# Kernel tuning notes

Hardware: AMD Instinct MI355X
Metric: run time of the kernel (lower is better)

Reference implementation:

```python
import jax, jax.numpy as jnp
import numpy as np

N, E, IN_DIM, HID, HEADS, LAYERS, NUM_STORES = 50000, 800000, 64, 128, 16, 3, 50
DH = HID // HEADS  # per-head dim = 8
EPS = 1e-5


def setup_inputs() -> dict:
    key = jax.random.key(0)
    ks = iter(jax.random.split(key, 40))
    def nrm(shape, scale):
        return jax.random.normal(next(ks), shape, dtype=jnp.float32) * scale
    inp = {}
    inp['x'] = jax.random.normal(next(ks), (N, IN_DIM), dtype=jnp.float32)
    inp['edge_index'] = jax.random.randint(next(ks), (2, E), 0, N, dtype=jnp.int32)
    inp['edge_weight'] = jax.random.uniform(next(ks), (E, 1), dtype=jnp.float32)
    inp['store_mask'] = jax.random.randint(next(ks), (N,), 0, NUM_STORES, dtype=jnp.int32)
    # input_proj: Linear + GELU + LayerNorm
    inp['in_W'] = nrm((IN_DIM, HID), IN_DIM ** -0.5)
    inp['in_b'] = jnp.zeros((HID,), jnp.float32)
    inp['in_g'] = jnp.ones((HID,), jnp.float32)
    inp['in_beta'] = jnp.zeros((HID,), jnp.float32)
    # 3 stacked GATv2 layers (stacked leading dim = layer)
    s = HID ** -0.5
    inp['gat_Wl'] = nrm((LAYERS, HID, HID), s)
    inp['gat_bl'] = jnp.zeros((LAYERS, HID), jnp.float32)
    inp['gat_Wr'] = nrm((LAYERS, HID, HID), s)
    inp['gat_br'] = jnp.zeros((LAYERS, HID), jnp.float32)
    inp['gat_We'] = nrm((LAYERS, 1, HID), 1.0)
    inp['gat_att'] = nrm((LAYERS, HEADS, DH), DH ** -0.5)
    inp['gat_bias'] = jnp.zeros((LAYERS, HID), jnp.float32)
    inp['blk_g'] = jnp.ones((LAYERS, HID), jnp.float32)
    inp['blk_b'] = jnp.zeros((LAYERS, HID), jnp.float32)
    # per-store context gate + final norm
    inp['ctx_W'] = nrm((HID, HID), s)
    inp['ctx_b'] = jnp.zeros((HID,), jnp.float32)
    inp['fin_g'] = jnp.ones((HID,), jnp.float32)
    inp['fin_b'] = jnp.zeros((HID,), jnp.float32)
    return inp


def layernorm(x, g, b):
    mu = jnp.mean(x, axis=-1, keepdims=True)
    v = jnp.mean((x - mu) ** 2, axis=-1, keepdims=True)
    return (x - mu) * jax.lax.rsqrt(v + EPS) * g + b


def gatv2_layer(x, src, dst, ea, Wl, bl, Wr, br, We, att, bias):
    # x: [N, HID]; src/dst: [Et]; ea: [Et, 1]
    n = x.shape[0]
    xl = (x @ Wl + bl).reshape(n, HEADS, DH)   # source transform
    xr = (x @ Wr + br).reshape(n, HEADS, DH)   # target transform
    ee = (ea @ We).reshape(-1, HEADS, DH)      # edge-attr embedding
    e = jax.nn.leaky_relu(xl[src] + xr[dst] + ee, 0.2)  # [Et, H, D]
    logit = jnp.einsum('ehd,hd->eh', e, att)             # [Et, H]
    # segment softmax over incoming edges of each target node
    mx = jax.ops.segment_max(logit, dst, num_segments=n)
    p = jnp.exp(logit - mx[dst])
    Z = jax.ops.segment_sum(p, dst, num_segments=n)
    alpha = p / (Z[dst] + 1e-16)
    msg = alpha[:, :, None] * xl[src]                    # [Et, H, D]
    agg = jax.ops.segment_sum(msg, dst, num_segments=n)  # [N, H, D]
    return agg.reshape(n, HEADS * DH) + bias


def forward(x, edge_index, edge_weight, store_mask, in_W, in_b, in_g, in_beta,
            gat_Wl, gat_bl, gat_Wr, gat_br, gat_We, gat_att, gat_bias,
            blk_g, blk_b, ctx_W, ctx_b, fin_g, fin_b):
    n = x.shape[0]
    h = layernorm(jax.nn.gelu(x @ in_W + in_b, approximate=False), in_g, in_beta)
    src, dst = edge_index[0], edge_index[1]
    # PyG add_self_loops with fill_value='mean': per-target mean of incoming edge attrs
    deg = jax.ops.segment_sum(jnp.ones(src.shape, h.dtype), dst, num_segments=n)
    loop_attr = jax.ops.segment_sum(edge_weight, dst, num_segments=n) / jnp.maximum(deg, 1.0)[:, None]
    loops = jnp.arange(n, dtype=src.dtype)
    srcf = jnp.concatenate([src, loops])
    dstf = jnp.concatenate([dst, loops])
    eaf = jnp.concatenate([edge_weight, loop_attr], axis=0)
    for l in range(LAYERS):  # residual block: post-norm residual around conv
        m = gatv2_layer(h, srcf, dstf, eaf, gat_Wl[l], gat_bl[l], gat_Wr[l], gat_br[l],
                        gat_We[l], gat_att[l], gat_bias[l])
        h = layernorm(h + m, blk_g[l], blk_b[l])
    # per-store segmented mean -> sigmoid gate -> scatter back
    cnt = jax.ops.segment_sum(jnp.ones((n,), h.dtype), store_mask, num_segments=NUM_STORES)
    means = jax.ops.segment_sum(h, store_mask, num_segments=NUM_STORES) / jnp.maximum(cnt, 1.0)[:, None]
    gate = jax.nn.sigmoid(means @ ctx_W + ctx_b)
    h = h + (gate * means)[store_mask]
    return layernorm(h, fin_g, fin_b)


def reference(x, edge_index, edge_weight, store_mask, in_W, in_b, in_g, in_beta,
              gat_Wl, gat_bl, gat_Wr, gat_br, gat_We, gat_att, gat_bias,
              blk_g, blk_b, ctx_W, ctx_b, fin_g, fin_b):
    return forward(x, edge_index, edge_weight, store_mask, in_W, in_b, in_g, in_beta,
                   gat_Wl, gat_bl, gat_Wr, gat_br, gat_We, gat_att, gat_bias,
                   blk_g, blk_b, ctx_W, ctx_b, fin_g, fin_b)
```

## Files before the change

kernel.cpp:

```cpp
#include <hip/hip_runtime.h>
#include <math.h>

#define NN 50000
#define EE 800000
#define ET (EE + NN)
#define HID 128
#define NSTORE 50
#define NBL 196
#define CNT_B 3125
#define XCV_B 3125
#define WCV_B 192
#define IWC_B 32
#define SCT_B 3321
#define GEMB 391
#define SSB 512

typedef unsigned short ushort_t;
typedef unsigned long long u64;
typedef __attribute__((ext_vector_type(8))) short bf8;
typedef __attribute__((ext_vector_type(4))) float f4;
typedef __attribute__((ext_vector_type(2))) float f2;
typedef __attribute__((ext_vector_type(4))) unsigned int u4;

__device__ __forceinline__ ushort_t f2b(float f) {
    union { float f; unsigned int i; } v; v.f = f;
    unsigned int r = (v.i + 0x7fffu + ((v.i >> 16) & 1u)) >> 16;
    return (ushort_t)r;
}
__device__ __forceinline__ f2 b2f2v(unsigned int u) {
    union { unsigned int i; float f; } lo, hi;
    lo.i = u << 16; hi.i = u & 0xffff0000u;
    f2 r; r.x = lo.f; r.y = hi.f; return r;
}
__device__ __forceinline__ unsigned int pk2(float lo, float hi) {
    return (unsigned int)f2b(lo) | ((unsigned int)f2b(hi) << 16);
}
__device__ __forceinline__ f2 max2(f2 a, f2 b) {
#if __has_builtin(__builtin_elementwise_max)
    return __builtin_elementwise_max(a, b);
#else
    f2 r; r.x = fmaxf(a.x, b.x); r.y = fmaxf(a.y, b.y); return r;
#endif
}

__global__ __launch_bounds__(256) void k_build(const int* __restrict__ ei, const float* __restrict__ ew,
                                               const float* __restrict__ x, const float* __restrict__ inW,
                                               const float* __restrict__ gWl, const float* __restrict__ gWr,
                                               ushort_t* __restrict__ xb, ushort_t* __restrict__ inWt,
                                               ushort_t* __restrict__ Wlt, ushort_t* __restrict__ Wrt,
                                               u64* __restrict__ packed, int* __restrict__ rank) {
    int b = blockIdx.x, t = threadIdx.x;
    if (b < CNT_B) {
        int i = b * 256 + t;
        int dst = ei[EE + i];
        unsigned int wfix = __float2uint_rn(ew[i] * 16777216.0f);
        u64 old = atomicAdd(&packed[dst], (1ULL << 44) | (u64)wfix);
        rank[i] = (int)(old >> 44);
        return;
    }
    if (b < CNT_B + XCV_B) {
        int i = ((b - CNT_B) * 256 + t) * 4;
        f4 v = *(const f4*)(x + i);
        uint2 p; p.x = pk2(v.x, v.y); p.y = pk2(v.z, v.w);
        *(uint2*)(xb + i) = p;
        return;
    }
    if (b < CNT_B + XCV_B + WCV_B) {
        int i = (b - CNT_B - XCV_B) * 256 + t;
        int l = i >> 14, r = i & 16383, nn2 = r >> 7, k = r & 127;
        Wlt[i] = f2b(gWl[(size_t)l * 16384 + k * 128 + nn2]);
        Wrt[i] = f2b(gWr[(size_t)l * 16384 + k * 128 + nn2]);
        return;
    }
    {
        int i = (b - CNT_B - XCV_B - WCV_B) * 256 + t;
        int c = i >> 6, k = i & 63;
        inWt[i] = f2b(inW[k * 128 + c]);
    }
}

__global__ __launch_bounds__(256) void k_inproj(const ushort_t* __restrict__ A,
                                                const ushort_t* __restrict__ Wt,
                                                const float* __restrict__ bias,
                                                const float* __restrict__ g,
                                                const float* __restrict__ be,
                                                ushort_t* __restrict__ hb) {
    const int K = 64;
    __shared__ float s1[2][128], s2[2][128];
    int lane = threadIdx.x & 63, w = threadIdx.x >> 6;
    int rw = w >> 1, cw = w & 1;
    int q = lane >> 4, l16 = lane & 15;
    int row0 = blockIdx.x * 128 + rw * 64;
    int col0 = cw * 64;
    bf8 z; for (int t = 0; t < 8; ++t) z[t] = 0;

    bf8 bfr[2][4];
#pragma unroll
    for (int kk = 0; kk < 2; ++kk)
#pragma unroll
        for (int j = 0; j < 4; ++j)
            bfr[kk][j] = *(const bf8*)(Wt + (size_t)(col0 + j * 16 + l16) * K + kk * 32 + q * 8);

    f4 acc[4][4];
#pragma unroll
    for (int i = 0; i < 4; ++i)
#pragma unroll
        for (int j = 0; j < 4; ++j) acc[i][j] = (f4)(0.f);

#pragma unroll
    for (int kk = 0; kk < 2; ++kk) {
        bf8 af[4];
#pragma unroll
        for (int i = 0; i < 4; ++i) {
            int r = row0 + i * 16 + l16;
            af[i] = (r < NN) ? *(const bf8*)(A + (size_t)r * K + kk * 32 + q * 8) : z;
        }
#pragma unroll
        for (int i = 0; i < 4; ++i)
#pragma unroll
            for (int j = 0; j < 4; ++j)
                acc[i][j] = __builtin_amdgcn_mfma_f32_16x16x32_bf16(af[i], bfr[kk][j], acc[i][j], 0, 0, 0);
    }
#pragma unroll
    for (int i = 0; i < 4; ++i) {
#pragma unroll
        for (int j = 0; j < 4; ++j) {
            float bv = bias[col0 + j * 16 + l16];
#pragma unroll
            for (int r = 0; r < 4; ++r) {
                float v = acc[i][j][r] + bv;
                v = 0.5f * v * (1.f + erff(v * 0.70710678118654752f));
                acc[i][j][r] = v;
            }
        }
    }
#pragma unroll
    for (int i = 0; i < 4; ++i) {
#pragma unroll
        for (int r = 0; r < 4; ++r) {
            float sm = acc[i][0][r] + acc[i][1][r] + acc[i][2][r] + acc[i][3][r];
            float sq = acc[i][0][r] * acc[i][0][r] + acc[i][1][r] * acc[i][1][r]
                     + acc[i][2][r] * acc[i][2][r] + acc[i][3][r] * acc[i][3][r];
#pragma unroll
            for (int k = 1; k < 16; k <<= 1) { sm += __shfl_xor(sm, k); sq += __shfl_xor(sq, k); }
            if (l16 == 0) {
                int rl = rw * 64 + i * 16 + q * 4 + r;
                s1[cw][rl] = sm; s2[cw][rl] = sq;
            }
        }
    }
    __syncthreads();
#pragma unroll
    for (int i = 0; i < 4; ++i) {
#pragma unroll
        for (int r = 0; r < 4; ++r) {
            int rl = rw * 64 + i * 16 + q * 4 + r;
            int gr = blockIdx.x * 128 + rl;
            if (gr >= NN) continue;
            float sm = s1[0][rl] + s1[1][rl];
            float sq = s2[0][rl] + s2[1][rl];
            float mu = sm * (1.f / 128.f);
            float var = sq * (1.f / 128.f) - mu * mu;
            float rinv = rsqrtf(var + 1e-5f);
#pragma unroll
            for (int j = 0; j < 4; ++j) {
                int gc = col0 + j * 16 + l16;
                float v = (acc[i][j][r] - mu) * rinv * g[gc] + be[gc];
                hb[(size_t)gr * HID + gc] = f2b(v);
            }
        }
    }
}

__global__ __launch_bounds__(256) void k_psum(const u64* __restrict__ packed, int* __restrict__ bsum) {
    int t = threadIdx.x, bidx = blockIdx.x;
    int i = bidx * 256 + t;
    int v = (i < NN) ? (int)(packed[i] >> 44) + 1 : 0;
#pragma unroll
    for (int d = 1; d < 64; d <<= 1) v += __shfl_xor(v, d);
    __shared__ int ws4[4];
    if ((t & 63) == 0) ws4[t >> 6] = v;
    __syncthreads();
    if (t == 0) bsum[bidx] = ws4[0] + ws4[1] + ws4[2] + ws4[3];
}

__global__ __launch_bounds__(256) void k_scanb(const int* __restrict__ bsum,
                                               int* __restrict__ bbase, int* __restrict__ offs) {
    __shared__ int s[256];
    int t = threadIdx.x;
    int v = (t < NBL) ? bsum[t] : 0;
    s[t] = v;
    __syncthreads();
    for (int d = 1; d < 256; d <<= 1) {
        int u = (t >= d) ? s[t - d] : 0;
        __syncthreads();
        s[t] += u;
        __syncthreads();
    }
    if (t < NBL) bbase[t] = s[t] - v;
    if (t == 0) offs[NN] = ET;
}

__global__ __launch_bounds__(256) void k_offs(const u64* __restrict__ packed,
                                              const int* __restrict__ bbase, int* __restrict__ offs) {
    __shared__ int wsum4[4];
    int t = threadIdx.x, bidx = blockIdx.x;
    int i = bidx * 256 + t;
    int v = (i < NN) ? (int)(packed[i] >> 44) + 1 : 0;
    int lane = t & 63, w = t >> 6;
    int sc = v;
#pragma unroll
    for (int d = 1; d < 64; d <<= 1) {
        int u = __shfl_up(sc, d);
        if (lane >= d) sc += u;
    }
    if (lane == 63) wsum4[w] = sc;
    __syncthreads();
    int wo = 0;
    for (int k = 0; k < w; ++k) wo += wsum4[k];
    if (i < NN) offs[i] = bbase[bidx] + wo + sc - v;
}

__global__ __launch_bounds__(256) void k_gemm2(const ushort_t* __restrict__ A,
                                               const ushort_t* __restrict__ Wt0,
                                               const ushort_t* __restrict__ Wt1,
                                               const float* __restrict__ b0,
                                               const float* __restrict__ b1,
                                               ushort_t* __restrict__ o0,
                                               ushort_t* __restrict__ o1, int n,
                                               const int* __restrict__ ei,
                                               const float* __restrict__ ew,
                                               const int* __restrict__ offs,
                                               const u64* __restrict__ packed,
                                               const int* __restrict__ rank,
                                               int2* __restrict__ csr) {
    int bid = blockIdx.x;
    if (bid >= 2 * GEMB) {
        int i = (bid - 2 * GEMB) * 256 + threadIdx.x;
        if (i < EE) {
            int src = ei[i], dst = ei[EE + i];
            int pos = offs[dst] + rank[i];
            int2 v; v.x = src << 8; v.y = __float_as_int(ew[i]);
            csr[pos] = v;
        } else if (i < ET) {
            int nd = i - EE;
            u64 p = packed[nd];
            int deg = (int)(p >> 44);
            float wsf = (float)(p & ((1ULL << 44) - 1)) * (1.0f / 16777216.0f);
            float la = wsf / fmaxf((float)deg, 1.0f);
            int pos = offs[nd + 1] - 1;
            int2 v; v.x = nd << 8; v.y = __float_as_int(la);
            csr[pos] = v;
        }
        return;
    }
    const int K = 128;
    int by = (bid >= GEMB) ? 1 : 0;
    int bx = by ? bid - GEMB : bid;
    const ushort_t* Wt = by ? Wt1 : Wt0;
    const float* bias = by ? b1 : b0;
    ushort_t* outb = by ? o1 : o0;
    int lane = threadIdx.x & 63, w = threadIdx.x >> 6;
    int rw = w >> 1, cw = w & 1;
    int q = lane >> 4, l16 = lane & 15;
    int row0 = bx * 128 + rw * 64;
    int col0 = cw * 64;
    bf8 z; for (int t = 0; t < 8; ++t) z[t] = 0;

    bf8 bfr[4][4];
#pragma unroll
    for (int kk = 0; kk < 4; ++kk)
#pragma unroll
        for (int j = 0; j < 4; ++j)
            bfr[kk][j] = *(const bf8*)(Wt + (size_t)(col0 + j * 16 + l16) * K + kk * 32 + q * 8);

    f4 acc[4][4];
#pragma unroll
    for (int i = 0; i < 4; ++i)
#pragma unroll
        for (int j = 0; j < 4; ++j) acc[i][j] = (f4)(0.f);

#pragma unroll
    for (int kk = 0; kk < 4; ++kk) {
        bf8 af[4];
#pragma unroll
        for (int i = 0; i < 4; ++i) {
            int r = row0 + i * 16 + l16;
            af[i] = (r < n) ? *(const bf8*)(A + (size_t)r * K + kk * 32 + q * 8) : z;
        }
#pragma unroll
        for (int i = 0; i < 4; ++i)
#pragma unroll
            for (int j = 0; j < 4; ++j)
                acc[i][j] = __builtin_amdgcn_mfma_f32_16x16x32_bf16(af[i], bfr[kk][j], acc[i][j], 0, 0, 0);
    }
#pragma unroll
    for (int i = 0; i < 4; ++i) {
        int gr0 = row0 + i * 16 + q * 4;
#pragma unroll
        for (int j = 0; j < 4; ++j) {
            int gc = col0 + j * 16 + l16;
            float bv = bias[gc];
#pragma unroll
            for (int r = 0; r < 4; ++r) {
                int gr = gr0 + r;
                if (gr < n) outb[(size_t)gr * HID + gc] = f2b(acc[i][j][r] + bv);
            }
        }
    }
}

__global__ __launch_bounds__(256) void k_attn(const ushort_t* __restrict__ xl,
                                              const ushort_t* __restrict__ xr,
                                              ushort_t* __restrict__ hb,
                                              const int* __restrict__ offs,
                                              const int2* __restrict__ csr,
                                              const float* __restrict__ We,
                                              const float* __restrict__ att,
                                              const float* __restrict__ gbias,
                                              const float* __restrict__ g,
                                              const float* __restrict__ b) {
    int wid = (blockIdx.x * 256 + threadIdx.x) >> 6;
    int lane = threadIdx.x & 63;
    if (wid >= NN) return;
    int hd = lane & 15;
    int grp = lane >> 4;
    int dbase = hd * 8;
    int db2 = hd * 16;
    size_t base = (size_t)wid * HID;

    f2 xr2[4], at2[4], we2[4];
    {
        u4 uxr = *(const u4*)(xr + base + dbase);
        xr2[0] = b2f2v(uxr.x); xr2[1] = b2f2v(uxr.y);
        xr2[2] = b2f2v(uxr.z); xr2[3] = b2f2v(uxr.w);
        f4 a0 = *(const f4*)(att + dbase), a1 = *(const f4*)(att + dbase + 4);
        at2[0].x = a0.x; at2[0].y = a0.y; at2[1].x = a0.z; at2[1].y = a0.w;
        at2[2].x = a1.x; at2[2].y = a1.y; at2[3].x = a1.z; at2[3].y = a1.w;
        f4 w0 = *(const f4*)(We + dbase), w1 = *(const f4*)(We + dbase + 4);
        we2[0].x = w0.x; we2[0].y = w0.y; we2[1].x = w0.z; we2[1].y = w0.w;
        we2[2].x = w1.x; we2[2].y = w1.y; we2[3].x = w1.z; we2[3].y = w1.w;
    }
    int p0 = offs[wid], p1 = offs[wid + 1];
    float Z = 0.f;
    f2 acc2[4];
#pragma unroll
    for (int q = 0; q < 4; ++q) { acc2[q].x = 0.f; acc2[q].y = 0.f; }

#define LOADQ(UX, EA, VM)                                                      \
    {                                                                          \
        int ei_ = e + grp;                                                     \
        VM = (ei_ < p1);                                                       \
        int2 m2_ = csr[VM ? ei_ : (p1 - 1)];                                   \
        EA = __int_as_float(m2_.y);                                            \
        UX = *(const u4*)((const char*)xl + (unsigned)m2_.x + db2);            \
    }

#define COMPQ(UX, EA, VM)                                                      \
    {                                                                          \
        f2 x2_[4];                                                             \
        x2_[0] = b2f2v(UX.x); x2_[1] = b2f2v(UX.y);                            \
        x2_[2] = b2f2v(UX.z); x2_[3] = b2f2v(UX.w);                            \
        f2 lg2_; lg2_.x = 0.f; lg2_.y = 0.f;                                   \
        _Pragma("unroll")                                                      \
        for (int q_ = 0; q_ < 4; ++q_) {                                       \
            f2 t_ = (x2_[q_] + xr2[q_]) + EA * we2[q_];                        \
            t_ = max2(t_, t_ * 0.2f);                                          \
            lg2_ += at2[q_] * t_;                                              \
        }                                                                      \
        float w_ = VM ? __expf(lg2_.x + lg2_.y) : 0.f;                         \
        Z += w_;                                                               \
        _Pragma("unroll")                                                      \
        for (int q_ = 0; q_ < 4; ++q_) acc2[q_] += w_ * x2_[q_];               \
    }

    {
        u4 uxA, uxB; float eaA, eaB; bool vA, vB;
        int e = p0;
        LOADQ(uxA, eaA, vA)
        e += 4;
        while (e < p1) {
            LOADQ(uxB, eaB, vB)
            e += 4;
            COMPQ(uxA, eaA, vA)
            if (e >= p1) { COMPQ(uxB, eaB, vB) goto redux; }
            LOADQ(uxA, eaA, vA)
            e += 4;
            COMPQ(uxB, eaB, vB)
        }
        COMPQ(uxA, eaA, vA)
    }
redux:;
#undef LOADQ
#undef COMPQ

    Z += __shfl_xor(Z, 16); Z += __shfl_xor(Z, 32);
#pragma unroll
    for (int q = 0; q < 4; ++q) {
        acc2[q].x += __shfl_xor(acc2[q].x, 16);
        acc2[q].x += __shfl_xor(acc2[q].x, 32);
        acc2[q].y += __shfl_xor(acc2[q].y, 16);
        acc2[q].y += __shfl_xor(acc2[q].y, 32);
    }
    float inv = 1.f / (Z + 1e-16f);
    float acc[8] = {acc2[0].x, acc2[0].y, acc2[1].x, acc2[1].y,
                    acc2[2].x, acc2[2].y, acc2[3].x, acc2[3].y};

    u4 uh = *(const u4*)(hb + base + dbase);
    f2 hr0 = b2f2v(uh.x), hr1 = b2f2v(uh.y), hr2 = b2f2v(uh.z), hr3 = b2f2v(uh.w);
    float hres[8] = {hr0.x, hr0.y, hr1.x, hr1.y, hr2.x, hr2.y, hr3.x, hr3.y};
    f4 gb0 = *(const f4*)(gbias + dbase), gb1 = *(const f4*)(gbias + dbase + 4);
    float gb8[8] = {gb0.x, gb0.y, gb0.z, gb0.w, gb1.x, gb1.y, gb1.z, gb1.w};
    float o[8], sm = 0.f, sq = 0.f;
#pragma unroll
    for (int q = 0; q < 8; ++q) {
        o[q] = acc[q] * inv + gb8[q] + hres[q];
        sm += o[q]; sq += o[q] * o[q];
    }
#pragma unroll
    for (int k = 1; k < 16; k <<= 1) { sm += __shfl_xor(sm, k); sq += __shfl_xor(sq, k); }
    float mu = sm * (1.f / 128.f);
    float var = sq * (1.f / 128.f) - mu * mu;
    float rinv = rsqrtf(var + 1e-5f);
    f4 g0 = *(const f4*)(g + dbase), g1 = *(const f4*)(g + dbase + 4);
    float g8[8] = {g0.x, g0.y, g0.z, g0.w, g1.x, g1.y, g1.z, g1.w};
    f4 b0 = *(const f4*)(b + dbase), b1 = *(const f4*)(b + dbase + 4);
    float b8[8] = {b0.x, b0.y, b0.z, b0.w, b1.x, b1.y, b1.z, b1.w};
    float v8[8];
#pragma unroll
    for (int q = 0; q < 8; ++q) v8[q] = (o[q] - mu) * rinv * g8[q] + b8[q];
    if (grp == 0) {
        u4 hu;
        hu.x = pk2(v8[0], v8[1]); hu.y = pk2(v8[2], v8[3]);
        hu.z = pk2(v8[4], v8[5]); hu.w = pk2(v8[6], v8[7]);
        *(u4*)(hb + base + dbase) = hu;
    }
}

__global__ __launch_bounds__(256) void k_store_sum(const ushort_t* __restrict__ hb,
                                                   const int* __restrict__ mask,
                                                   float* __restrict__ psums,
                                                   int* __restrict__ pcnts) {
    __shared__ float ls[NSTORE * HID];
    __shared__ int lc[NSTORE];
    int t = threadIdx.x, bidx = blockIdx.x;
    for (int i = t; i < NSTORE * HID; i += 256) ls[i] = 0.f;
    if (t < NSTORE) lc[t] = 0;
    __syncthreads();
    int wid = bidx * 4 + (t >> 6);
    int lane = t & 63;
    int nw = SSB * 4;
    int d0 = lane * 2;
    for (int node = wid; node < NN; node += nw) {
        int s = mask[node];
        unsigned int hv = ((const unsigned int*)(hb + (size_t)node * HID))[lane];
        f2 v = b2f2v(hv);
        atomicAdd(&ls[s * HID + d0], v.x);
        atomicAdd(&ls[s * HID + d0 + 1], v.y);
        if (lane == 0) atomicAdd(&lc[s], 1);
    }
    __syncthreads();
    for (int i = t; i < NSTORE * HID; i += 256) psums[(size_t)bidx * (NSTORE * HID) + i] = ls[i];
    if (t < NSTORE) pcnts[bidx * NSTORE + t] = lc[t];
}

__global__ __launch_bounds__(256) void k_gate(const float* __restrict__ psums,
                                              const int* __restrict__ pcnts,
                                              const float* __restrict__ ctxW,
                                              const float* __restrict__ ctxb,
                                              float* __restrict__ gm) {
    __shared__ float h1[HID];
    __shared__ float mloc[HID];
    __shared__ int cw4[4];
    int s = blockIdx.x, t = threadIdx.x;
    int d = t & 127, half = t >> 7;
    float s0 = 0.f, s1 = 0.f, s2 = 0.f, s3 = 0.f;
    for (int b = half * 4; b < SSB; b += 8) {
        s0 += psums[(size_t)(b + 0) * (NSTORE * HID) + s * HID + d];
        s1 += psums[(size_t)(b + 1) * (NSTORE * HID) + s * HID + d];
        s2 += psums[(size_t)(b + 2) * (NSTORE * HID) + s * HID + d];
        s3 += psums[(size_t)(b + 3) * (NSTORE * HID) + s * HID + d];
    }
    float sum = (s0 + s1) + (s2 + s3);
    int c = pcnts[t * NSTORE + s] + pcnts[(t + 256) * NSTORE + s];
#pragma unroll
    for (int k = 1; k < 64; k <<= 1) c += __shfl_xor(c, k);
    if ((t & 63) == 0) cw4[t >> 6] = c;
    if (half) h1[d] = sum;
    __syncthreads();
    if (half == 0) {
        float tot = sum + h1[d];
        float cnt = fmaxf((float)(cw4[0] + cw4[1] + cw4[2] + cw4[3]), 1.f);
        mloc[d] = tot / cnt;
    }
    __syncthreads();
    if (half == 0) {
        float acc = ctxb[d];
        for (int j = 0; j < HID; ++j) acc += mloc[j] * ctxW[j * HID + d];
        float gate = 1.f / (1.f + __expf(-acc));
        gm[s * HID + d] = gate * mloc[d];
    }
}

__global__ __launch_bounds__(256) void k_final(const ushort_t* __restrict__ hb,
                                               const int* __restrict__ mask,
                                               const float* __restrict__ gm,
                                               const float* __restrict__ g,
                                               const float* __restrict__ b,
                                               float* __restrict__ out) {
    int wid = (blockIdx.x * 256 + threadIdx.x) >> 6;
    int lane = threadIdx.x & 63;
    if (wid >= NN) return;
    size_t base = (size_t)wid * HID;
    int s = mask[wid];
    int d0 = lane * 2, d1 = d0 + 1;
    unsigned int hv = ((const unsigned int*)(hb + base))[lane];
    f2 hvv = b2f2v(hv);
    float v0 = hvv.x + gm[s * HID + d0];
    float v1 = hvv.y + gm[s * HID + d1];
    float sm = v0 + v1, sq = v0 * v0 + v1 * v1;
#pragma unroll
    for (int k = 1; k < 64; k <<= 1) { sm += __shfl_xor(sm, k); sq += __shfl_xor(sq, k); }
    float mu = sm * (1.f / 128.f);
    float var = sq * (1.f / 128.f) - mu * mu;
    float r = rsqrtf(var + 1e-5f);
    out[base + d0] = (v0 - mu) * r * g[d0] + b[d0];
    out[base + d1] = (v1 - mu) * r * g[d1] + b[d1];
}

extern "C" void kernel_launch(void* const* d_in, const int* in_sizes, int n_in,
                              void* d_out, int out_size, void* d_ws, size_t ws_size,
                              hipStream_t stream) {
    const float* x      = (const float*)d_in[0];
    const int*   ei     = (const int*)d_in[1];
    const float* ew     = (const float*)d_in[2];
    const int*   smask  = (const int*)d_in[3];
    const float* inW    = (const float*)d_in[4];
    const float* inb    = (const float*)d_in[5];
    const float* ing    = (const float*)d_in[6];
    const float* inbeta = (const float*)d_in[7];
    const float* gWl    = (const float*)d_in[8];
    const float* gbl    = (const float*)d_in[9];
    const float* gWr    = (const float*)d_in[10];
    const float* gbr    = (const float*)d_in[11];
    const float* gWe    = (const float*)d_in[12];
    const float* gatt   = (const float*)d_in[13];
    const float* gbias  = (const float*)d_in[14];
    const float* blkg   = (const float*)d_in[15];
    const float* blkb   = (const float*)d_in[16];
    const float* ctxW   = (const float*)d_in[17];
    const float* ctxb   = (const float*)d_in[18];
    const float* fing   = (const float*)d_in[19];
    const float* finb   = (const float*)d_in[20];
    float* out = (float*)d_out;

    float* ws = (float*)d_ws;
    size_t o = 0;
    int2*     csr    = (int2*)(ws + o);     o += (size_t)ET * 2;
    float*    gm     = ws + o;              o += NSTORE * HID;
    int*      offs   = (int*)(ws + o);      o += 50004;
    int*      rank   = (int*)(ws + o);      o += EE;
    ushort_t* xb     = (ushort_t*)(ws + o); o += (size_t)NN * 64 / 2;
    ushort_t* hb     = (ushort_t*)(ws + o); o += (size_t)NN * HID / 2;
    ushort_t* xlb    = (ushort_t*)(ws + o); o += (size_t)NN * HID / 2;
    ushort_t* xrb    = (ushort_t*)(ws + o); o += (size_t)NN * HID / 2;
    ushort_t* inWt   = (ushort_t*)(ws + o); o += 128 * 64 / 2;
    ushort_t* Wlt    = (ushort_t*)(ws + o); o += 3 * 128 * 128 / 2;
    ushort_t* Wrt    = (ushort_t*)(ws + o); o += 3 * 128 * 128 / 2;
    int*      bsum   = (int*)(ws + o);      o += 256;
    int*      bbase  = (int*)(ws + o);      o += 256;
    float*    psums  = ws + o;              o += (size_t)SSB * NSTORE * HID;
    int*      pcnts  = (int*)(ws + o);      o += SSB * NSTORE;
    if (o & 1) ++o;
    float*    zbase  = ws + o;
    u64*      packed = (u64*)(ws + o);      o += (size_t)NN * 2;
    size_t zbytes = (size_t)(NN * 2) * 4;

    hipMemsetAsync((void*)zbase, 0, zbytes, stream);

    const int WB = NN / 4;

    k_build<<<CNT_B + XCV_B + WCV_B + IWC_B, 256, 0, stream>>>(ei, ew, x, inW, gWl, gWr,
                                                               xb, inWt, Wlt, Wrt, packed, rank);
    k_inproj<<<GEMB, 256, 0, stream>>>(xb, inWt, inb, ing, inbeta, hb);
    k_psum<<<NBL, 256, 0, stream>>>(packed, bsum);
    k_scanb<<<1, 256, 0, stream>>>(bsum, bbase, offs);
    k_offs<<<NBL, 256, 0, stream>>>(packed, bbase, offs);

    for (int l = 0; l < 3; ++l) {
        int nb = 2 * GEMB + (l == 0 ? SCT_B : 0);
        k_gemm2<<<nb, 256, 0, stream>>>(hb, Wlt + (size_t)l * HID * HID, Wrt + (size_t)l * HID * HID,
                                        gbl + l * HID, gbr + l * HID, xlb, xrb, NN,
                                        ei, ew, offs, packed, rank, csr);
        k_attn<<<WB, 256, 0, stream>>>(xlb, xrb, hb, offs, csr,
                                       gWe + l * HID, gatt + l * HID, gbias + l * HID,
                                       blkg + l * HID, blkb + l * HID);
    }

    k_store_sum<<<SSB, 256, 0, stream>>>(hb, smask, psums, pcnts);
    k_gate<<<NSTORE, 256, 0, stream>>>(psums, pcnts, ctxW, ctxb, gm);
    k_final<<<WB, 256, 0, stream>>>(hb, smask, gm, fing, finb, out);
}
```

Before: 507.6 us.

## Batch CSR record loads via lane shuffles and make attention kernel persistent

The attention kernel becomes grid-stride persistent with a fixed grid, and its launch bounds now request 8 waves per SIMD. Each wave loads up to 64 CSR records for its node in a single coalesced load and hands them out with shuffles. It then issues up to four gathers of neighbour features before computing, instead of one CSR load followed by a dependent gather. This removes the serial CSR-then-gather latency chain and increases memory-level parallelism. The costs are more registers, a fallback loop for nodes with degree above 64, and a grid-stride loop that may balance load unevenly.

```diff
diff --git a/kernel.cpp b/kernel.cpp
--- a/kernel.cpp
+++ b/kernel.cpp
@@ -14,6 +14,7 @@
 #define SCT_B 3321
 #define GEMB 391
 #define SSB 512
+#define ATT_B 2048
 
 typedef unsigned short ushort_t;
 typedef unsigned long long u64;
@@ -310,30 +311,25 @@
     }
 }
 
-__global__ __launch_bounds__(256) void k_attn(const ushort_t* __restrict__ xl,
-                                              const ushort_t* __restrict__ xr,
-                                              ushort_t* __restrict__ hb,
-                                              const int* __restrict__ offs,
-                                              const int2* __restrict__ csr,
-                                              const float* __restrict__ We,
-                                              const float* __restrict__ att,
-                                              const float* __restrict__ gbias,
-                                              const float* __restrict__ g,
-                                              const float* __restrict__ b) {
-    int wid = (blockIdx.x * 256 + threadIdx.x) >> 6;
+__global__ __launch_bounds__(256, 8) void k_attn(const ushort_t* __restrict__ xl,
+                                                 const ushort_t* __restrict__ xr,
+                                                 ushort_t* __restrict__ hb,
+                                                 const int* __restrict__ offs,
+                                                 const int2* __restrict__ csr,
+                                                 const float* __restrict__ We,
+                                                 const float* __restrict__ att,
+                                                 const float* __restrict__ gbias,
+                                                 const float* __restrict__ g,
+                                                 const float* __restrict__ b) {
     int lane = threadIdx.x & 63;
-    if (wid >= NN) return;
+    int wslot = __builtin_amdgcn_readfirstlane(threadIdx.x >> 6);
     int hd = lane & 15;
     int grp = lane >> 4;
     int dbase = hd * 8;
     int db2 = hd * 16;
-    size_t base = (size_t)wid * HID;
-
-    f2 xr2[4], at2[4], we2[4];
+
+    f2 at2[4], we2[4];
     {
-        u4 uxr = *(const u4*)(xr + base + dbase);
-        xr2[0] = b2f2v(uxr.x); xr2[1] = b2f2v(uxr.y);
-        xr2[2] = b2f2v(uxr.z); xr2[3] = b2f2v(uxr.w);
         f4 a0 = *(const f4*)(att + dbase), a1 = *(const f4*)(att + dbase + 4);
         at2[0].x = a0.x; at2[0].y = a0.y; at2[1].x = a0.z; at2[1].y = a0.w;
         at2[2].x = a1.x; at2[2].y = a1.y; at2[3].x = a1.z; at2[3].y = a1.w;
@@ -341,23 +337,37 @@
         we2[0].x = w0.x; we2[0].y = w0.y; we2[1].x = w0.z; we2[1].y = w0.w;
         we2[2].x = w1.x; we2[2].y = w1.y; we2[3].x = w1.z; we2[3].y = w1.w;
     }
-    int p0 = offs[wid], p1 = offs[wid + 1];
-    float Z = 0.f;
-    f2 acc2[4];
-#pragma unroll
-    for (int q = 0; q < 4; ++q) { acc2[q].x = 0.f; acc2[q].y = 0.f; }
-
-#define LOADQ(UX, EA, VM)                                                      \
+
+    for (int wid = blockIdx.x * 4 + wslot; wid < NN; wid += ATT_B * 4) {
+        size_t base = (size_t)wid * HID;
+        f2 xr2[4];
+        {
+            u4 uxr = *(const u4*)(xr + base + dbase);
+            xr2[0] = b2f2v(uxr.x); xr2[1] = b2f2v(uxr.y);
+            xr2[2] = b2f2v(uxr.z); xr2[3] = b2f2v(uxr.w);
+        }
+        int p0 = offs[wid], p1 = offs[wid + 1];
+        int deg = p1 - p0;
+        int nmain = deg > 64 ? 64 : deg;
+        int2 rec = csr[p0 + ((lane < deg) ? lane : deg - 1)];
+
+        float Z = 0.f;
+        f2 acc2[4];
+#pragma unroll
+        for (int q = 0; q < 4; ++q) { acc2[q].x = 0.f; acc2[q].y = 0.f; }
+
+#define ISSUE(K, UX, EA)                                                       \
     {                                                                          \
-        int ei_ = e + grp;                                                     \
-        VM = (ei_ < p1);                                                       \
-        int2 m2_ = csr[VM ? ei_ : (p1 - 1)];                                   \
-        EA = __int_as_float(m2_.y);                                            \
-        UX = *(const u4*)((const char*)xl + (unsigned)m2_.x + db2);            \
-    }
-
-#define COMPQ(UX, EA, VM)                                                      \
+        int ie_ = e0 + 4 * K + grp;                                            \
+        int is_ = (ie_ < nmain) ? ie_ : 0;                                     \
+        EA = __int_as_float(__shfl(rec.y, is_));                               \
+        int sx_ = __shfl(rec.x, is_);                                          \
+        UX = *(const u4*)((const char*)xl + (unsigned)sx_ + db2);              \
+    }
+
+#define COMP(K, UX, EA)                                                        \
     {                                                                          \
+        bool vm_ = (e0 + 4 * K + grp) < nmain;                                 \
         f2 x2_[4];                                                             \
         x2_[0] = b2f2v(UX.x); x2_[1] = b2f2v(UX.y);                            \
         x2_[2] = b2f2v(UX.z); x2_[3] = b2f2v(UX.w);                            \
@@ -368,72 +378,91 @@
             t_ = max2(t_, t_ * 0.2f);                                          \
             lg2_ += at2[q_] * t_;                                              \
         }                                                                      \
-        float w_ = VM ? __expf(lg2_.x + lg2_.y) : 0.f;                         \
+        float w_ = vm_ ? __expf(lg2_.x + lg2_.y) : 0.f;                        \
         Z += w_;                                                               \
         _Pragma("unroll")                                                      \
         for (int q_ = 0; q_ < 4; ++q_) acc2[q_] += w_ * x2_[q_];               \
     }
 
-    {
-        u4 uxA, uxB; float eaA, eaB; bool vA, vB;
-        int e = p0;
-        LOADQ(uxA, eaA, vA)
-        e += 4;
-        while (e < p1) {
-            LOADQ(uxB, eaB, vB)
-            e += 4;
-            COMPQ(uxA, eaA, vA)
-            if (e >= p1) { COMPQ(uxB, eaB, vB) goto redux; }
-            LOADQ(uxA, eaA, vA)
-            e += 4;
-            COMPQ(uxB, eaB, vB)
-        }
-        COMPQ(uxA, eaA, vA)
-    }
-redux:;
-#undef LOADQ
-#undef COMPQ
-
-    Z += __shfl_xor(Z, 16); Z += __shfl_xor(Z, 32);
-#pragma unroll
-    for (int q = 0; q < 4; ++q) {
-        acc2[q].x += __shfl_xor(acc2[q].x, 16);
-        acc2[q].x += __shfl_xor(acc2[q].x, 32);
-        acc2[q].y += __shfl_xor(acc2[q].y, 16);
-        acc2[q].y += __shfl_xor(acc2[q].y, 32);
-    }
-    float inv = 1.f / (Z + 1e-16f);
-    float acc[8] = {acc2[0].x, acc2[0].y, acc2[1].x, acc2[1].y,
-                    acc2[2].x, acc2[2].y, acc2[3].x, acc2[3].y};
-
-    u4 uh = *(const u4*)(hb + base + dbase);
-    f2 hr0 = b2f2v(uh.x), hr1 = b2f2v(uh.y), hr2 = b2f2v(uh.z), hr3 = b2f2v(uh.w);
-    float hres[8] = {hr0.x, hr0.y, hr1.x, hr1.y, hr2.x, hr2.y, hr3.x, hr3.y};
-    f4 gb0 = *(const f4*)(gbias + dbase), gb1 = *(const f4*)(gbias + dbase + 4);
-    float gb8[8] = {gb0.x, gb0.y, gb0.z, gb0.w, gb1.x, gb1.y, gb1.z, gb1.w};
-    float o[8], sm = 0.f, sq = 0.f;
-#pragma unroll
-    for (int q = 0; q < 8; ++q) {
-        o[q] = acc[q] * inv + gb8[q] + hres[q];
-        sm += o[q]; sq += o[q] * o[q];
-    }
-#pragma unroll
-    for (int k = 1; k < 16; k <<= 1) { sm += __shfl_xor(sm, k); sq += __shfl_xor(sq, k); }
-    float mu = sm * (1.f / 128.f);
-    float var = sq * (1.f / 128.f) - mu * mu;
-    float rinv = rsqrtf(var + 1e-5f);
-    f4 g0 = *(const f4*)(g + dbase), g1 = *(const f4*)(g + dbase + 4);
-    float g8[8] = {g0.x, g0.y, g0.z, g0.w, g1.x, g1.y, g1.z, g1.w};
-    f4 b0 = *(const f4*)(b + dbase), b1 = *(const f4*)(b + dbase + 4);
-    float b8[8] = {b0.x, b0.y, b0.z, b0.w, b1.x, b1.y, b1.z, b1.w};
-    float v8[8];
-#pragma unroll
-    for (int q = 0; q < 8; ++q) v8[q] = (o[q] - mu) * rinv * g8[q] + b8[q];
-    if (grp == 0) {
-        u4 hu;
-        hu.x = pk2(v8[0], v8[1]); hu.y = pk2(v8[2], v8[3]);
-        hu.z = pk2(v8[4], v8[5]); hu.w = pk2(v8[6], v8[7]);
-        *(u4*)(hb + base + dbase) = hu;
+        for (int e0 = 0; e0 < nmain; e0 += 16) {
+            int nr = nmain - e0;
+            u4 uxA, uxB, uxC, uxD;
+            float eaA, eaB, eaC, eaD;
+            ISSUE(0, uxA, eaA)
+            if (nr > 4)  ISSUE(1, uxB, eaB)
+            if (nr > 8)  ISSUE(2, uxC, eaC)
+            if (nr > 12) ISSUE(3, uxD, eaD)
+            COMP(0, uxA, eaA)
+            if (nr > 4)  COMP(1, uxB, eaB)
+            if (nr > 8)  COMP(2, uxC, eaC)
+            if (nr > 12) COMP(3, uxD, eaD)
+        }
+#undef ISSUE
+#undef COMP
+
+        for (int e = p0 + 64; e < p1; e += 4) {
+            int ei_ = e + grp;
+            bool vm_ = ei_ < p1;
+            int2 m2_ = csr[vm_ ? ei_ : p1 - 1];
+            float ea_ = __int_as_float(m2_.y);
+            u4 ux_ = *(const u4*)((const char*)xl + (unsigned)m2_.x + db2);
+            f2 x2_[4];
+            x2_[0] = b2f2v(ux_.x); x2_[1] = b2f2v(ux_.y);
+            x2_[2] = b2f2v(ux_.z); x2_[3] = b2f2v(ux_.w);
+            f2 lg2_; lg2_.x = 0.f; lg2_.y = 0.f;
+#pragma unroll
+            for (int q_ = 0; q_ < 4; ++q_) {
+                f2 t_ = (x2_[q_] + xr2[q_]) + ea_ * we2[q_];
+                t_ = max2(t_, t_ * 0.2f);
+                lg2_ += at2[q_] * t_;
+            }
+            float w_ = vm_ ? __expf(lg2_.x + lg2_.y) : 0.f;
+            Z += w_;
+#pragma unroll
+            for (int q_ = 0; q_ < 4; ++q_) acc2[q_] += w_ * x2_[q_];
+        }
+
+        Z += __shfl_xor(Z, 16); Z += __shfl_xor(Z, 32);
+#pragma unroll
+        for (int q = 0; q < 4; ++q) {
+            acc2[q].x += __shfl_xor(acc2[q].x, 16);
+            acc2[q].x += __shfl_xor(acc2[q].x, 32);
+            acc2[q].y += __shfl_xor(acc2[q].y, 16);
+            acc2[q].y += __shfl_xor(acc2[q].y, 32);
+        }
+        float inv = 1.f / (Z + 1e-16f);
+        float acc[8] = {acc2[0].x, acc2[0].y, acc2[1].x, acc2[1].y,
+                        acc2[2].x, acc2[2].y, acc2[3].x, acc2[3].y};
+
+        u4 uh = *(const u4*)(hb + base + dbase);
+        f2 hr0 = b2f2v(uh.x), hr1 = b2f2v(uh.y), hr2 = b2f2v(uh.z), hr3 = b2f2v(uh.w);
+        float hres[8] = {hr0.x, hr0.y, hr1.x, hr1.y, hr2.x, hr2.y, hr3.x, hr3.y};
+        f4 gb0 = *(const f4*)(gbias + dbase), gb1 = *(const f4*)(gbias + dbase + 4);
+        float gb8[8] = {gb0.x, gb0.y, gb0.z, gb0.w, gb1.x, gb1.y, gb1.z, gb1.w};
+        float o[8], sm = 0.f, sq = 0.f;
+#pragma unroll
+        for (int q = 0; q < 8; ++q) {
+            o[q] = acc[q] * inv + gb8[q] + hres[q];
+            sm += o[q]; sq += o[q] * o[q];
+        }
+#pragma unroll
+        for (int k = 1; k < 16; k <<= 1) { sm += __shfl_xor(sm, k); sq += __shfl_xor(sq, k); }
+        float mu = sm * (1.f / 128.f);
+        float var = sq * (1.f / 128.f) - mu * mu;
+        float rinv = rsqrtf(var + 1e-5f);
+        f4 g0 = *(const f4*)(g + dbase), g1 = *(const f4*)(g + dbase + 4);
+        float g8[8] = {g0.x, g0.y, g0.z, g0.w, g1.x, g1.y, g1.z, g1.w};
+        f4 b0 = *(const f4*)(b + dbase), b1 = *(const f4*)(b + dbase + 4);
+        float b8[8] = {b0.x, b0.y, b0.z, b0.w, b1.x, b1.y, b1.z, b1.w};
+        float v8[8];
+#pragma unroll
+        for (int q = 0; q < 8; ++q) v8[q] = (o[q] - mu) * rinv * g8[q] + b8[q];
+        if (grp == 0) {
+            u4 hu;
+            hu.x = pk2(v8[0], v8[1]); hu.y = pk2(v8[2], v8[3]);
+            hu.z = pk2(v8[4], v8[5]); hu.w = pk2(v8[6], v8[7]);
+            *(u4*)(hb + base + dbase) = hu;
+        }
     }
 }
 
@@ -592,9 +621,9 @@
         k_gemm2<<<nb, 256, 0, stream>>>(hb, Wlt + (size_t)l * HID * HID, Wrt + (size_t)l * HID * HID,
                                         gbl + l * HID, gbr + l * HID, xlb, xrb, NN,
                                         ei, ew, offs, packed, rank, csr);
-        k_attn<<<WB, 256, 0, stream>>>(xlb, xrb, hb, offs, csr,
-                                       gWe + l * HID, gatt + l * HID, gbias + l * HID,
-                                       blkg + l * HID, blkb + l * HID);
+        k_attn<<<ATT_B, 256, 0, stream>>>(xlb, xrb, hb, offs, csr,
+                                          gWe + l * HID, gatt + l * HID, gbias + l * HID,
+                                          blkg + l * HID, blkb + l * HID);
     }
 
     k_store_sum<<<SSB, 256, 0, stream>>>(hb, smask, psums, pcnts);
```

Result: slower. 856.2 us (+68.7%).

## Fuse x bf16 conversion into inproj, merge scan kernels, share A tile in gemm2

Applied to the files above, without the earlier changes.

Drops the separate x-to-bf16 conversion pass and converts fp32 inputs to bf16 on the fly inside the input projection GEMM. Replaces the single-block scan plus offsets kernels with one kernel where each block reduces the preceding block sums itself, removing a launch. Reworks the layer GEMM into 512-thread blocks that stage the 128-row A tile once in swizzled LDS and compute both the Wl and Wr outputs from it, halving A reads from global. The CSR scatter tail is resized to match. Weight fragments are now loaded per k-step instead of all up front.

```diff
diff --git a/kernel.cpp b/kernel.cpp
--- a/kernel.cpp
+++ b/kernel.cpp
@@ -8,10 +8,9 @@
 #define NSTORE 50
 #define NBL 196
 #define CNT_B 3125
-#define XCV_B 3125
 #define WCV_B 192
 #define IWC_B 32
-#define SCT_B 3321
+#define SCT_B2 1661
 #define GEMB 391
 #define SSB 512
 
@@ -44,9 +43,9 @@
 }
 
 __global__ __launch_bounds__(256) void k_build(const int* __restrict__ ei, const float* __restrict__ ew,
-                                               const float* __restrict__ x, const float* __restrict__ inW,
+                                               const float* __restrict__ inW,
                                                const float* __restrict__ gWl, const float* __restrict__ gWr,
-                                               ushort_t* __restrict__ xb, ushort_t* __restrict__ inWt,
+                                               ushort_t* __restrict__ inWt,
                                                ushort_t* __restrict__ Wlt, ushort_t* __restrict__ Wrt,
                                                u64* __restrict__ packed, int* __restrict__ rank) {
     int b = blockIdx.x, t = threadIdx.x;
@@ -58,28 +57,21 @@
         rank[i] = (int)(old >> 44);
         return;
     }
-    if (b < CNT_B + XCV_B) {
-        int i = ((b - CNT_B) * 256 + t) * 4;
-        f4 v = *(const f4*)(x + i);
-        uint2 p; p.x = pk2(v.x, v.y); p.y = pk2(v.z, v.w);
-        *(uint2*)(xb + i) = p;
-        return;
-    }
-    if (b < CNT_B + XCV_B + WCV_B) {
-        int i = (b - CNT_B - XCV_B) * 256 + t;
+    if (b < CNT_B + WCV_B) {
+        int i = (b - CNT_B) * 256 + t;
         int l = i >> 14, r = i & 16383, nn2 = r >> 7, k = r & 127;
         Wlt[i] = f2b(gWl[(size_t)l * 16384 + k * 128 + nn2]);
         Wrt[i] = f2b(gWr[(size_t)l * 16384 + k * 128 + nn2]);
         return;
     }
     {
-        int i = (b - CNT_B - XCV_B - WCV_B) * 256 + t;
+        int i = (b - CNT_B - WCV_B) * 256 + t;
         int c = i >> 6, k = i & 63;
         inWt[i] = f2b(inW[k * 128 + c]);
     }
 }
 
-__global__ __launch_bounds__(256) void k_inproj(const ushort_t* __restrict__ A,
+__global__ __launch_bounds__(256) void k_inproj(const float* __restrict__ X,
                                                 const ushort_t* __restrict__ Wt,
                                                 const float* __restrict__ bias,
                                                 const float* __restrict__ g,
@@ -113,7 +105,14 @@
 #pragma unroll
         for (int i = 0; i < 4; ++i) {
             int r = row0 + i * 16 + l16;
-            af[i] = (r < NN) ? *(const bf8*)(A + (size_t)r * K + kk * 32 + q * 8) : z;
+            if (r < NN) {
+                const float* xp = X + (size_t)r * K + kk * 32 + q * 8;
+                f4 a = *(const f4*)xp;
+                f4 c = *(const f4*)(xp + 4);
+                u4 up; up.x = pk2(a.x, a.y); up.y = pk2(a.z, a.w);
+                up.z = pk2(c.x, c.y); up.w = pk2(c.z, c.w);
+                af[i] = *(bf8*)&up;
+            } else af[i] = z;
         }
 #pragma unroll
         for (int i = 0; i < 4; ++i)
@@ -184,30 +183,20 @@
     if (t == 0) bsum[bidx] = ws4[0] + ws4[1] + ws4[2] + ws4[3];
 }
 
-__global__ __launch_bounds__(256) void k_scanb(const int* __restrict__ bsum,
-                                               int* __restrict__ bbase, int* __restrict__ offs) {
-    __shared__ int s[256];
-    int t = threadIdx.x;
-    int v = (t < NBL) ? bsum[t] : 0;
-    s[t] = v;
-    __syncthreads();
-    for (int d = 1; d < 256; d <<= 1) {
-        int u = (t >= d) ? s[t - d] : 0;
-        __syncthreads();
-        s[t] += u;
-        __syncthreads();
-    }
-    if (t < NBL) bbase[t] = s[t] - v;
-    if (t == 0) offs[NN] = ET;
-}
-
-__global__ __launch_bounds__(256) void k_offs(const u64* __restrict__ packed,
-                                              const int* __restrict__ bbase, int* __restrict__ offs) {
+__global__ __launch_bounds__(256) void k_offs2(const u64* __restrict__ packed,
+                                               const int* __restrict__ bsum, int* __restrict__ offs) {
+    __shared__ int bws[4];
     __shared__ int wsum4[4];
     int t = threadIdx.x, bidx = blockIdx.x;
     int i = bidx * 256 + t;
     int v = (i < NN) ? (int)(packed[i] >> 44) + 1 : 0;
     int lane = t & 63, w = t >> 6;
+
+    int bv = (t < bidx) ? bsum[t] : 0;
+#pragma unroll
+    for (int d = 1; d < 64; d <<= 1) bv += __shfl_xor(bv, d);
+    if (lane == 0) bws[w] = bv;
+
     int sc = v;
 #pragma unroll
     for (int d = 1; d < 64; d <<= 1) {
@@ -216,12 +205,14 @@
     }
     if (lane == 63) wsum4[w] = sc;
     __syncthreads();
+    int base = bws[0] + bws[1] + bws[2] + bws[3];
     int wo = 0;
     for (int k = 0; k < w; ++k) wo += wsum4[k];
-    if (i < NN) offs[i] = bbase[bidx] + wo + sc - v;
-}
-
-__global__ __launch_bounds__(256) void k_gemm2(const ushort_t* __restrict__ A,
+    if (i < NN) offs[i] = base + wo + sc - v;
+    if (bidx == 0 && t == 0) offs[NN] = ET;
+}
+
+__global__ __launch_bounds__(512) void k_gemm2(const ushort_t* __restrict__ A,
                                                const ushort_t* __restrict__ Wt0,
                                                const ushort_t* __restrict__ Wt1,
                                                const float* __restrict__ b0,
@@ -235,8 +226,8 @@
                                                const int* __restrict__ rank,
                                                int2* __restrict__ csr) {
     int bid = blockIdx.x;
-    if (bid >= 2 * GEMB) {
-        int i = (bid - 2 * GEMB) * 256 + threadIdx.x;
+    if (bid >= GEMB) {
+        int i = (bid - GEMB) * 512 + threadIdx.x;
         if (i < EE) {
             int src = ei[i], dst = ei[EE + i];
             int pos = offs[dst] + rank[i];
@@ -255,48 +246,60 @@
         return;
     }
     const int K = 128;
-    int by = (bid >= GEMB) ? 1 : 0;
-    int bx = by ? bid - GEMB : bid;
-    const ushort_t* Wt = by ? Wt1 : Wt0;
-    const float* bias = by ? b1 : b0;
-    ushort_t* outb = by ? o1 : o0;
-    int lane = threadIdx.x & 63, w = threadIdx.x >> 6;
-    int rw = w >> 1, cw = w & 1;
+    __shared__ char As[128 * 256];
+    int t = threadIdx.x;
+    int row0 = bid * 128;
+    bf8 z; for (int k = 0; k < 8; ++k) z[k] = 0;
+
+    {
+        int row = t >> 2, cq = t & 3;
+        const ushort_t* srcp = A + (size_t)(row0 + row) * K + cq * 8;
+        int swz = (row & 7) << 4;
+        char* dst = As + row * 256;
+        bool ok = (row0 + row) < n;
+#pragma unroll
+        for (int k = 0; k < 4; ++k) {
+            bf8 v = ok ? *(const bf8*)(srcp + k * 32) : z;
+            *(bf8*)(dst + ((k * 64 + cq * 16) ^ swz)) = v;
+        }
+    }
+    __syncthreads();
+
+    int w = t >> 6, lane = t & 63;
+    int side = w >> 2, rw = (w >> 1) & 1, cw = w & 1;
+    const ushort_t* Wt = side ? Wt1 : Wt0;
+    const float* bias = side ? b1 : b0;
+    ushort_t* outb = side ? o1 : o0;
     int q = lane >> 4, l16 = lane & 15;
-    int row0 = bx * 128 + rw * 64;
     int col0 = cw * 64;
-    bf8 z; for (int t = 0; t < 8; ++t) z[t] = 0;
-
-    bf8 bfr[4][4];
-#pragma unroll
-    for (int kk = 0; kk < 4; ++kk)
+
+    f4 acc[4][4];
+#pragma unroll
+    for (int i = 0; i < 4; ++i)
+#pragma unroll
+        for (int j = 0; j < 4; ++j) acc[i][j] = (f4)(0.f);
+
+#pragma unroll
+    for (int kk = 0; kk < 4; ++kk) {
+        bf8 bfk[4];
 #pragma unroll
         for (int j = 0; j < 4; ++j)
-            bfr[kk][j] = *(const bf8*)(Wt + (size_t)(col0 + j * 16 + l16) * K + kk * 32 + q * 8);
-
-    f4 acc[4][4];
-#pragma unroll
-    for (int i = 0; i < 4; ++i)
-#pragma unroll
-        for (int j = 0; j < 4; ++j) acc[i][j] = (f4)(0.f);
-
-#pragma unroll
-    for (int kk = 0; kk < 4; ++kk) {
+            bfk[j] = *(const bf8*)(Wt + (size_t)(col0 + j * 16 + l16) * K + kk * 32 + q * 8);
         bf8 af[4];
 #pragma unroll
         for (int i = 0; i < 4; ++i) {
-            int r = row0 + i * 16 + l16;
-            af[i] = (r < n) ? *(const bf8*)(A + (size_t)r * K + kk * 32 + q * 8) : z;
+            int r = rw * 64 + i * 16 + l16;
+            af[i] = *(const bf8*)(As + r * 256 + ((kk * 64 + q * 16) ^ ((r & 7) << 4)));
         }
 #pragma unroll
         for (int i = 0; i < 4; ++i)
 #pragma unroll
             for (int j = 0; j < 4; ++j)
-                acc[i][j] = __builtin_amdgcn_mfma_f32_16x16x32_bf16(af[i], bfr[kk][j], acc[i][j], 0, 0, 0);
+                acc[i][j] = __builtin_amdgcn_mfma_f32_16x16x32_bf16(af[i], bfk[j], acc[i][j], 0, 0, 0);
     }
 #pragma unroll
     for (int i = 0; i < 4; ++i) {
-        int gr0 = row0 + i * 16 + q * 4;
+        int gr0 = row0 + rw * 64 + i * 16 + q * 4;
 #pragma unroll
         for (int j = 0; j < 4; ++j) {
             int gc = col0 + j * 16 + l16;
@@ -560,7 +563,6 @@
     float*    gm     = ws + o;              o += NSTORE * HID;
     int*      offs   = (int*)(ws + o);      o += 50004;
     int*      rank   = (int*)(ws + o);      o += EE;
-    ushort_t* xb     = (ushort_t*)(ws + o); o += (size_t)NN * 64 / 2;
     ushort_t* hb     = (ushort_t*)(ws + o); o += (size_t)NN * HID / 2;
     ushort_t* xlb    = (ushort_t*)(ws + o); o += (size_t)NN * HID / 2;
     ushort_t* xrb    = (ushort_t*)(ws + o); o += (size_t)NN * HID / 2;
@@ -568,7 +570,6 @@
     ushort_t* Wlt    = (ushort_t*)(ws + o); o += 3 * 128 * 128 / 2;
     ushort_t* Wrt    = (ushort_t*)(ws + o); o += 3 * 128 * 128 / 2;
     int*      bsum   = (int*)(ws + o);      o += 256;
-    int*      bbase  = (int*)(ws + o);      o += 256;
     float*    psums  = ws + o;              o += (size_t)SSB * NSTORE * HID;
     int*      pcnts  = (int*)(ws + o);      o += SSB * NSTORE;
     if (o & 1) ++o;
@@ -580,16 +581,15 @@
 
     const int WB = NN / 4;
 
-    k_build<<<CNT_B + XCV_B + WCV_B + IWC_B, 256, 0, stream>>>(ei, ew, x, inW, gWl, gWr,
-                                                               xb, inWt, Wlt, Wrt, packed, rank);
-    k_inproj<<<GEMB, 256, 0, stream>>>(xb, inWt, inb, ing, inbeta, hb);
+    k_build<<<CNT_B + WCV_B + IWC_B, 256, 0, stream>>>(ei, ew, inW, gWl, gWr,
+                                                       inWt, Wlt, Wrt, packed, rank);
+    k_inproj<<<GEMB, 256, 0, stream>>>(x, inWt, inb, ing, inbeta, hb);
     k_psum<<<NBL, 256, 0, stream>>>(packed, bsum);
-    k_scanb<<<1, 256, 0, stream>>>(bsum, bbase, offs);
-    k_offs<<<NBL, 256, 0, stream>>>(packed, bbase, offs);
+    k_offs2<<<NBL, 256, 0, stream>>>(packed, bsum, offs);
 
     for (int l = 0; l < 3; ++l) {
-        int nb = 2 * GEMB + (l == 0 ? SCT_B : 0);
-        k_gemm2<<<nb, 256, 0, stream>>>(hb, Wlt + (size_t)l * HID * HID, Wrt + (size_t)l * HID * HID,
+        int nb = GEMB + (l == 0 ? SCT_B2 : 0);
+        k_gemm2<<<nb, 512, 0, stream>>>(hb, Wlt + (size_t)l * HID * HID, Wrt + (size_t)l * HID * HID,
                                         gbl + l * HID, gbr + l * HID, xlb, xrb, NN,
                                         ei, ew, offs, packed, rank, csr);
         k_attn<<<WB, 256, 0, stream>>>(xlb, xrb, hb, offs, csr,
```

Measured after the change: 475.4 us. 1.07x faster.
